# Optimization experiments

Measured on AMD Instinct MI355X. Metric: run time of the kernel, lower is better.

Reference implementation:

```python
import jax, jax.numpy as jnp
import numpy as np

B, N, D, H, C = 4, 1024, 768, 12, 3
Dh = D // H                      # 64
HID = int(D * 4.0 * (2.0 / 3.0)) # 2048 (SwiGLU hidden)
EPS = 1e-5


def layernorm(x, g, b):
    m = jnp.mean(x, axis=-1, keepdims=True)
    v = jnp.mean(jnp.square(x - m), axis=-1, keepdims=True)
    return (x - m) * jax.lax.rsqrt(v + EPS) * g + b


def setup_inputs() -> dict:
    key = jax.random.key(0)
    ks = jax.random.split(key, 8)
    x = jax.random.normal(ks[0], (B, N, D), jnp.float32)
    coords = jax.random.uniform(ks[1], (B, N, C), jnp.float32)
    qkv_w = jax.random.normal(ks[2], (3 * D, D), jnp.float32) * 0.02
    qkv_b = jnp.zeros((3 * D,), jnp.float32)
    rel_w = jax.random.normal(ks[3], (H, C), jnp.float32) * 0.1
    ln1_g = jnp.ones((D,), jnp.float32)
    ln1_b = jnp.zeros((D,), jnp.float32)
    ln2_g = jnp.ones((D,), jnp.float32)
    ln2_b = jnp.zeros((D,), jnp.float32)
    win_w = jax.random.normal(ks[4], (2 * HID, D), jnp.float32) * 0.02
    win_b = jnp.zeros((2 * HID,), jnp.float32)
    wout_w = jax.random.normal(ks[5], (D, HID), jnp.float32) * 0.02
    wout_b = jnp.zeros((D,), jnp.float32)
    return dict(x=x, coords=coords, ln1_g=ln1_g, ln1_b=ln1_b, qkv_w=qkv_w,
                qkv_b=qkv_b, rel_w=rel_w, ln2_g=ln2_g, ln2_b=ln2_b,
                win_w=win_w, win_b=win_b, wout_w=wout_w, wout_b=wout_b)


def reference(x, coords, ln1_g, ln1_b, qkv_w, qkv_b, rel_w, ln2_g, ln2_b,
              win_w, win_b, wout_w, wout_b):
    # --- PatchAttention on norm1(x) ---
    h = layernorm(x, ln1_g, ln1_b)
    qkv = h @ qkv_w.T + qkv_b                    # (B,N,3D)
    q, k, v = jnp.split(qkv, 3, axis=-1)

    def heads(t):  # (B,N,D) -> (B,H,N,Dh)
        return t.reshape(B, N, H, Dh).transpose(0, 2, 1, 3)

    qh, kh, vh = heads(q), heads(k), heads(v)
    scale = 1.0 / np.sqrt(Dh).astype(np.float32)
    scores = jnp.einsum('bhid,bhjd->bhij', qh, kh) * scale
    # coord bias: (coords_i - coords_j) . W_h  ==  p[b,h,i] - p[b,h,j]
    p = jnp.einsum('bnc,hc->bhn', coords, rel_w)  # (B,H,N)
    scores = scores + p[:, :, :, None] - p[:, :, None, :]
    attn = jax.nn.softmax(scores, axis=-1)
    o = jnp.einsum('bhij,bhjd->bhid', attn, vh)   # (B,H,N,Dh)
    o = o.transpose(0, 2, 1, 3).reshape(B, N, D)
    x = x + o

    # --- SwiGLU FFN on norm2(x) ---
    h2 = layernorm(x, ln2_g, ln2_b)
    uv = h2 @ win_w.T + win_b                     # (B,N,2*HID)
    u, g = jnp.split(uv, 2, axis=-1)
    act = jax.nn.silu(u) * g
    return x + act @ wout_w.T + wout_b
```

## Files before the change

kernel.cpp:

```cpp
#include <hip/hip_runtime.h>
#include <math.h>

typedef unsigned short u16;
typedef __bf16 bf16x8 __attribute__((ext_vector_type(8)));
typedef __bf16 bf16x4 __attribute__((ext_vector_type(4)));
typedef u16 u16x4 __attribute__((ext_vector_type(4)));
typedef float f32x4 __attribute__((ext_vector_type(4)));

#define NTOK 1024
#define DMODEL 768
#define NHEAD 12
#define LD3 2304
#define HIDDIM 2048

__device__ __forceinline__ float b2f(u16 u) {
  unsigned int t = ((unsigned int)u) << 16;
  float f;
  __builtin_memcpy(&f, &t, 4);
  return f;
}
__device__ __forceinline__ u16 f2b(float f) {
  unsigned int t;
  __builtin_memcpy(&t, &f, 4);
  t += 0x7fffu + ((t >> 16) & 1u);
  return (u16)(t >> 16);
}

__device__ __forceinline__ void gl_lds16(const u16* g, u16* l) {
  __builtin_amdgcn_global_load_lds(
      (__attribute__((address_space(1))) const unsigned int*)g,
      (__attribute__((address_space(3))) unsigned int*)l, 16, 0, 0);
}

__global__ __launch_bounds__(256) void signal_kernel(float* __restrict__ out,
                                                     int n, float c) {
  int i = blockIdx.x * 256 + threadIdx.x;
  if (i < n) out[i] = c;
}

__global__ __launch_bounds__(256) void detect_kernel(const u16* __restrict__ x,
                                                     int* __restrict__ flag) {
  __shared__ int cnt;
  if (threadIdx.x == 0) cnt = 0;
  __syncthreads();
  int bad = 0;
  for (int i = threadIdx.x; i < 4096; i += 256) {
    u16 v = x[2 * i];
    int e = (v >> 7) & 0xFF;
    if (e >= 0xC0) bad++;
  }
  atomicAdd(&cnt, bad);
  __syncthreads();
  if (threadIdx.x == 0) *flag = (cnt >= 64) ? 1 : 0;
}

struct CanonJobs {
  const void* s[13];
  u16* d[13];
  int n[13];
};

__global__ __launch_bounds__(256) void canon_kernel(CanonJobs jobs,
                                                    const int* __restrict__ flag) {
  int j = blockIdx.y;
  int n4 = jobs.n[j] >> 2;
  const void* s = jobs.s[j];
  u16* d = jobs.d[j];
  bool isf32 = (*flag != 0);
  for (int i = blockIdx.x * 256 + threadIdx.x; i < n4; i += gridDim.x * 256) {
    if (isf32) {
      f32x4 v = *((const f32x4*)s + i);
      u16x4 o = {f2b(v[0]), f2b(v[1]), f2b(v[2]), f2b(v[3])};
      *((u16x4*)d + i) = o;
    } else {
      *((u16x4*)d + i) = *((const u16x4*)s + i);
    }
  }
}

__global__ __launch_bounds__(256) void ln_bf16_kernel(
    const u16* __restrict__ x, const u16* __restrict__ g,
    const u16* __restrict__ b, u16* __restrict__ out) {
  int row = blockIdx.x;
  int tid = threadIdx.x;
  const u16* xr = x + (size_t)row * DMODEL;
  float v0 = b2f(xr[tid]), v1 = b2f(xr[tid + 256]), v2 = b2f(xr[tid + 512]);
  float s = v0 + v1 + v2;
  float q = v0 * v0 + v1 * v1 + v2 * v2;
#pragma unroll
  for (int off = 32; off; off >>= 1) {
    s += __shfl_xor(s, off, 64);
    q += __shfl_xor(q, off, 64);
  }
  __shared__ float rs[4], rq[4];
  int wv = tid >> 6;
  if ((tid & 63) == 0) { rs[wv] = s; rq[wv] = q; }
  __syncthreads();
  s = rs[0] + rs[1] + rs[2] + rs[3];
  q = rq[0] + rq[1] + rq[2] + rq[3];
  float mean = s * (1.0f / 768.0f);
  float var = q * (1.0f / 768.0f) - mean * mean;
  float inv = rsqrtf(var + 1e-5f);
  u16* outr = out + (size_t)row * DMODEL;
  outr[tid]       = f2b((v0 - mean) * inv * b2f(g[tid])       + b2f(b[tid]));
  outr[tid + 256] = f2b((v1 - mean) * inv * b2f(g[tid + 256]) + b2f(b[tid + 256]));
  outr[tid + 512] = f2b((v2 - mean) * inv * b2f(g[tid + 512]) + b2f(b[tid + 512]));
}

__global__ __launch_bounds__(256) void ln_f32_kernel(
    const float* __restrict__ x, const u16* __restrict__ g,
    const u16* __restrict__ b, u16* __restrict__ out) {
  int row = blockIdx.x;
  int tid = threadIdx.x;
  const float* xr = x + (size_t)row * DMODEL;
  float v0 = xr[tid], v1 = xr[tid + 256], v2 = xr[tid + 512];
  float s = v0 + v1 + v2;
  float q = v0 * v0 + v1 * v1 + v2 * v2;
#pragma unroll
  for (int off = 32; off; off >>= 1) {
    s += __shfl_xor(s, off, 64);
    q += __shfl_xor(q, off, 64);
  }
  __shared__ float rs[4], rq[4];
  int wv = tid >> 6;
  if ((tid & 63) == 0) { rs[wv] = s; rq[wv] = q; }
  __syncthreads();
  s = rs[0] + rs[1] + rs[2] + rs[3];
  q = rq[0] + rq[1] + rq[2] + rq[3];
  float mean = s * (1.0f / 768.0f);
  float var = q * (1.0f / 768.0f) - mean * mean;
  float inv = rsqrtf(var + 1e-5f);
  u16* outr = out + (size_t)row * DMODEL;
  outr[tid]       = f2b((v0 - mean) * inv * b2f(g[tid])       + b2f(b[tid]));
  outr[tid + 256] = f2b((v1 - mean) * inv * b2f(g[tid + 256]) + b2f(b[tid + 256]));
  outr[tid + 512] = f2b((v2 - mean) * inv * b2f(g[tid + 512]) + b2f(b[tid + 512]));
}

__global__ __launch_bounds__(256) void gemm_bt(
    const u16* __restrict__ Ap, const u16* __restrict__ Wp,
    const u16* __restrict__ bias, u16* __restrict__ Cp, int Nn, int K) {
  __shared__ __align__(16) u16 Al[3 * 128 * 32], Bl[3 * 64 * 32];
  int lane = threadIdx.x & 63;
  int wv = threadIdx.x >> 6;
  int q16 = lane & 15, quad = lane >> 4;
  int mB0 = blockIdx.y * 128;
  int nB0 = blockIdx.x * 64;
  int mW = (wv >> 1) * 64, nW = (wv & 1) * 32;
  int srow = lane >> 2;
  int scol = ((lane & 3) ^ ((lane >> 3) & 3)) * 8;
  int sx8 = (quad ^ ((q16 >> 1) & 3)) * 8;
  int r0 = wv * 32 + srow, r1 = r0 + 16;
  int rb = wv * 16 + srow;
  const u16* Ag0 = Ap + (size_t)(mB0 + r0) * K + scol;
  const u16* Ag1 = Ap + (size_t)(mB0 + r1) * K + scol;
  const u16* Wg  = Wp + (size_t)(nB0 + rb) * K + scol;
  int ch0 = wv * 1024, ch1 = ch0 + 512, chb = wv * 512;
  int nsteps = K >> 5;
  f32x4 acc[4][2] = {};
#pragma unroll
  for (int tt = 0; tt < 2; ++tt) {
    int k0 = tt * 32;
    gl_lds16(Ag0 + k0, Al + tt * 4096 + ch0);
    gl_lds16(Ag1 + k0, Al + tt * 4096 + ch1);
    gl_lds16(Wg + k0, Bl + tt * 2048 + chb);
  }
  int n3 = nsteps / 3;
  for (int kb = 0; kb < n3; ++kb) {
#pragma unroll
    for (int c = 0; c < 3; ++c) {
      int t = kb * 3 + c;
      if (t < nsteps - 1) asm volatile("s_waitcnt vmcnt(3)" ::: "memory");
      else                asm volatile("s_waitcnt vmcnt(0)" ::: "memory");
      __builtin_amdgcn_sched_barrier(0);
      __builtin_amdgcn_s_barrier();
      __builtin_amdgcn_sched_barrier(0);
      if (t < nsteps - 2) {
        int k0 = (t + 2) * 32;
        int bs = (c + 2) % 3;
        gl_lds16(Ag0 + k0, Al + bs * 4096 + ch0);
        gl_lds16(Ag1 + k0, Al + bs * 4096 + ch1);
        gl_lds16(Wg + k0, Bl + bs * 2048 + chb);
      }
      const __bf16* Ab = (const __bf16*)(Al + c * 4096);
      const __bf16* Bb = (const __bf16*)(Bl + c * 2048);
      bf16x8 af[4], bfr[2];
#pragma unroll
      for (int si = 0; si < 4; ++si)
        af[si] = *(const bf16x8*)(Ab + (mW + si * 16 + q16) * 32 + sx8);
#pragma unroll
      for (int sj = 0; sj < 2; ++sj)
        bfr[sj] = *(const bf16x8*)(Bb + (nW + sj * 16 + q16) * 32 + sx8);
#pragma unroll
      for (int si = 0; si < 4; ++si)
#pragma unroll
        for (int sj = 0; sj < 2; ++sj)
          acc[si][sj] = __builtin_amdgcn_mfma_f32_16x16x32_bf16(af[si], bfr[sj], acc[si][sj], 0, 0, 0);
    }
  }
#pragma unroll
  for (int si = 0; si < 4; ++si)
#pragma unroll
    for (int sj = 0; sj < 2; ++sj) {
      int col = nB0 + nW + sj * 16 + q16;
      float bcol = b2f(bias[col]);
#pragma unroll
      for (int r = 0; r < 4; ++r) {
        int rowi = mB0 + mW + si * 16 + quad * 4 + r;
        Cp[(size_t)rowi * Nn + col] = f2b(acc[si][sj][r] + bcol);
      }
    }
}

__global__ __launch_bounds__(256) void gemm_out_split(
    const u16* __restrict__ Ap, const u16* __restrict__ Wp,
    const u16* __restrict__ bias, const float* __restrict__ res,
    float* __restrict__ part, float* __restrict__ out) {
  __shared__ __align__(16) u16 Al[4 * 128 * 32], Bl[4 * 64 * 32];
  int lane = threadIdx.x & 63;
  int wv = threadIdx.x >> 6;
  int q16 = lane & 15, quad = lane >> 4;
  int mB0 = blockIdx.y * 128;
  int nB0 = blockIdx.x * 64;
  int kz = blockIdx.z;
  int kbase = kz * 1024;
  int mW = (wv >> 1) * 64, nW = (wv & 1) * 32;
  int srow = lane >> 2;
  int scol = ((lane & 3) ^ ((lane >> 3) & 3)) * 8;
  int sx8 = (quad ^ ((q16 >> 1) & 3)) * 8;
  int r0 = wv * 32 + srow, r1 = r0 + 16;
  int rb = wv * 16 + srow;
  const u16* Ag0 = Ap + (size_t)(mB0 + r0) * 2048 + kbase + scol;
  const u16* Ag1 = Ap + (size_t)(mB0 + r1) * 2048 + kbase + scol;
  const u16* Wg  = Wp + (size_t)(nB0 + rb) * 2048 + kbase + scol;
  int ch0 = wv * 1024, ch1 = ch0 + 512, chb = wv * 512;
  f32x4 acc[4][2] = {};
#pragma unroll
  for (int tt = 0; tt < 2; ++tt) {
    int k0 = tt * 32;
    gl_lds16(Ag0 + k0, Al + tt * 4096 + ch0);
    gl_lds16(Ag1 + k0, Al + tt * 4096 + ch1);
    gl_lds16(Wg + k0, Bl + tt * 2048 + chb);
  }
  for (int kb = 0; kb < 8; ++kb) {
#pragma unroll
    for (int c = 0; c < 4; ++c) {
      int t = kb * 4 + c;
      if (t < 31) asm volatile("s_waitcnt vmcnt(3)" ::: "memory");
      else        asm volatile("s_waitcnt vmcnt(0)" ::: "memory");
      __builtin_amdgcn_sched_barrier(0);
      __builtin_amdgcn_s_barrier();
      __builtin_amdgcn_sched_barrier(0);
      if (t < 30) {
        int k0 = (t + 2) * 32;
        int bs = (c + 2) & 3;
        gl_lds16(Ag0 + k0, Al + bs * 4096 + ch0);
        gl_lds16(Ag1 + k0, Al + bs * 4096 + ch1);
        gl_lds16(Wg + k0, Bl + bs * 2048 + chb);
      }
      const __bf16* Ab = (const __bf16*)(Al + c * 4096);
      const __bf16* Bb = (const __bf16*)(Bl + c * 2048);
      bf16x8 af[4], bfr[2];
#pragma unroll
      for (int si = 0; si < 4; ++si)
        af[si] = *(const bf16x8*)(Ab + (mW + si * 16 + q16) * 32 + sx8);
#pragma unroll
      for (int sj = 0; sj < 2; ++sj)
        bfr[sj] = *(const bf16x8*)(Bb + (nW + sj * 16 + q16) * 32 + sx8);
#pragma unroll
      for (int si = 0; si < 4; ++si)
#pragma unroll
        for (int sj = 0; sj < 2; ++sj)
          acc[si][sj] = __builtin_amdgcn_mfma_f32_16x16x32_bf16(af[si], bfr[sj], acc[si][sj], 0, 0, 0);
    }
  }
#pragma unroll
  for (int si = 0; si < 4; ++si)
#pragma unroll
    for (int sj = 0; sj < 2; ++sj) {
      int col = nB0 + nW + sj * 16 + q16;
#pragma unroll
      for (int r = 0; r < 4; ++r) {
        int rowi = mB0 + mW + si * 16 + quad * 4 + r;
        size_t idx = (size_t)rowi * 768 + col;
        if (kz == 0) {
          part[idx] = acc[si][sj][r];
        } else {
          out[idx] = acc[si][sj][r] + b2f(bias[col]) + res[idx];
        }
      }
    }
}

__global__ __launch_bounds__(256) void add_kernel(float* __restrict__ out,
                                                  const float* __restrict__ part) {
  int i = blockIdx.x * 256 + threadIdx.x;
  f32x4 o = ((f32x4*)out)[i];
  f32x4 p = ((const f32x4*)part)[i];
#pragma unroll
  for (int r = 0; r < 4; ++r) o[r] += p[r];
  ((f32x4*)out)[i] = o;
}

__global__ __launch_bounds__(256) void ffn_in_kernel(
    const u16* __restrict__ hp, const u16* __restrict__ Wp,
    const u16* __restrict__ bias, u16* __restrict__ actp) {
  __shared__ __align__(16) u16 Al[3 * 128 * 32], Bl[3 * 64 * 32];
  int lane = threadIdx.x & 63;
  int wv = threadIdx.x >> 6;
  int q16 = lane & 15, quad = lane >> 4;
  int mB0 = blockIdx.y * 128;
  int cB0 = blockIdx.x * 32;
  int mW = (wv >> 1) * 64;
  int cW = (wv & 1) * 16;
  int srow = lane >> 2;
  int scol = ((lane & 3) ^ ((lane >> 3) & 3)) * 8;
  int sx8 = (quad ^ ((q16 >> 1) & 3)) * 8;
  int r0 = wv * 32 + srow, r1 = r0 + 16;
  int rb = wv * 16 + srow;
  int gb = (rb < 32) ? (cB0 + rb) : (HIDDIM + cB0 + rb - 32);
  const u16* Ag0 = hp + (size_t)(mB0 + r0) * DMODEL + scol;
  const u16* Ag1 = hp + (size_t)(mB0 + r1) * DMODEL + scol;
  const u16* Wg  = Wp + (size_t)gb * DMODEL + scol;
  int ch0 = wv * 1024, ch1 = ch0 + 512, chb = wv * 512;
  f32x4 au[4] = {}, ag[4] = {};
#pragma unroll
  for (int tt = 0; tt < 2; ++tt) {
    int k0 = tt * 32;
    gl_lds16(Ag0 + k0, Al + tt * 4096 + ch0);
    gl_lds16(Ag1 + k0, Al + tt * 4096 + ch1);
    gl_lds16(Wg + k0, Bl + tt * 2048 + chb);
  }
  for (int kb = 0; kb < 8; ++kb) {
#pragma unroll
    for (int c = 0; c < 3; ++c) {
      int t = kb * 3 + c;
      if (t < 23) asm volatile("s_waitcnt vmcnt(3)" ::: "memory");
      else        asm volatile("s_waitcnt vmcnt(0)" ::: "memory");
      __builtin_amdgcn_sched_barrier(0);
      __builtin_amdgcn_s_barrier();
      __builtin_amdgcn_sched_barrier(0);
      if (t < 22) {
        int k0 = (t + 2) * 32;
        int bs = (c + 2) % 3;
        gl_lds16(Ag0 + k0, Al + bs * 4096 + ch0);
        gl_lds16(Ag1 + k0, Al + bs * 4096 + ch1);
        gl_lds16(Wg + k0, Bl + bs * 2048 + chb);
      }
      const __bf16* Ab = (const __bf16*)(Al + c * 4096);
      const __bf16* Bb = (const __bf16*)(Bl + c * 2048);
      bf16x8 af[4], wu, wg;
#pragma unroll
      for (int si = 0; si < 4; ++si)
        af[si] = *(const bf16x8*)(Ab + (mW + si * 16 + q16) * 32 + sx8);
      wu = *(const bf16x8*)(Bb + (cW + q16) * 32 + sx8);
      wg = *(const bf16x8*)(Bb + (32 + cW + q16) * 32 + sx8);
#pragma unroll
      for (int si = 0; si < 4; ++si) {
        au[si] = __builtin_amdgcn_mfma_f32_16x16x32_bf16(af[si], wu, au[si], 0, 0, 0);
        ag[si] = __builtin_amdgcn_mfma_f32_16x16x32_bf16(af[si], wg, ag[si], 0, 0, 0);
      }
    }
  }
  int col = cB0 + cW + q16;
  float bu = b2f(bias[col]);
  float bg = b2f(bias[HIDDIM + col]);
#pragma unroll
  for (int si = 0; si < 4; ++si) {
#pragma unroll
    for (int r = 0; r < 4; ++r) {
      int rowi = mB0 + mW + si * 16 + quad * 4 + r;
      float u = au[si][r] + bu;
      float g = ag[si][r] + bg;
      float s = u / (1.0f + __expf(-u));
      actp[(size_t)rowi * HIDDIM + col] = f2b(s * g);
    }
  }
}

__global__ __launch_bounds__(256) void p_kernel(
    const u16* __restrict__ coords, const u16* __restrict__ relw,
    float* __restrict__ p) {
  const float LOG2E = 1.4426950408889634f;
  int idx = blockIdx.x * 256 + threadIdx.x;
  float c0 = b2f(coords[idx * 3 + 0]);
  float c1 = b2f(coords[idx * 3 + 1]);
  float c2 = b2f(coords[idx * 3 + 2]);
  int b = idx >> 10, n = idx & 1023;
#pragma unroll
  for (int h = 0; h < NHEAD; ++h) {
    float w0 = b2f(relw[h * 3 + 0]), w1 = b2f(relw[h * 3 + 1]), w2 = b2f(relw[h * 3 + 2]);
    p[(size_t)(b * NHEAD + h) * NTOK + n] = (c0 * w0 + c1 * w1 + c2 * w2) * LOG2E;
  }
}

__global__ __launch_bounds__(256) void vt_kernel(const u16* __restrict__ qkvp,
                                                 u16* __restrict__ vtp) {
  int blk = blockIdx.x;
  int b = blk / 192;
  int rem = blk % 192;
  int h = rem >> 4;
  int nt = rem & 15;
  int wv = threadIdx.x >> 6;
  int d = threadIdx.x & 63;
  int n0 = nt * 64 + wv * 16;
  const u16* src = qkvp + ((size_t)(b * NTOK) + n0) * LD3 + 2 * DMODEL + h * 64 + d;
  u16* dst = vtp + ((size_t)((b * NHEAD + h) * 64 + d)) * NTOK + n0;
#pragma unroll
  for (int c = 0; c < 2; ++c) {
    u16 buf[8] __attribute__((aligned(16)));
#pragma unroll
    for (int i = 0; i < 8; ++i) buf[i] = src[(size_t)(c * 8 + i) * LD3];
    *(uint4*)(dst + c * 8) = *(const uint4*)buf;
  }
}

__global__ __launch_bounds__(256) void attn_kernel(
    const u16* __restrict__ qkvp, const u16* __restrict__ vtp,
    const float* __restrict__ p2, const u16* __restrict__ xp,
    float* __restrict__ x1) {
  const __bf16* qb = (const __bf16*)qkvp;
  __shared__ __align__(16) u16 Kl[4][32 * 64];
  __shared__ __align__(16) u16 Vl[4][64 * 32];
  __shared__ __align__(16) u16 Pl[4][16][40];
  __shared__ __align__(16) float Pb[1024];
  int lane = threadIdx.x & 63;
  int wv = threadIdx.x >> 6;
  int hw = blockIdx.x;
  int g = hw % 48;
  int nt = hw / 48;
  int b = g / 12, h = g % 12;
  int i0 = (nt * 4 + wv) * 16;
  int q16 = lane & 15, quad = lane >> 4;

  const float scl2 = 0.125f * 1.4426950408889634f;

  const __bf16* qrow = qb + ((size_t)(b * NTOK) + i0 + q16) * LD3 + h * 64;
  bf16x8 bq0 = *(const bf16x8*)(qrow + quad * 8);
  bf16x8 bq1 = *(const bf16x8*)(qrow + 32 + quad * 8);

  const float* prow = p2 + (size_t)(b * NHEAD + h) * NTOK;

  int krw = wv * 8 + (lane >> 3);
  int ks  = (lane & 7) ^ (krw & 7);
  const u16* kg0 = qkvp + (size_t)(b * NTOK) * LD3 + DMODEL + h * 64 + ks * 8;
  int vrw = wv * 16 + (lane >> 2);
  int vs  = (lane & 3) ^ ((vrw >> 1) & 3);
  const u16* vg0 = vtp + ((size_t)((b * NHEAD + h) * 64 + vrw)) * NTOK + vs * 8;

  int kx0 = (quad ^ (q16 & 7)) << 3;
  int kx1 = ((4 | quad) ^ (q16 & 7)) << 3;
  int vx  = (quad ^ ((q16 >> 1) & 3)) << 3;

  float mrun = -1e30f, lsum = 0.f;
  f32x4 accO[4] = {};

  gl_lds16((const u16*)(prow + wv * 256 + lane * 4), (u16*)&Pb[wv * 256]);
#pragma unroll
  for (int tt = 0; tt < 3; ++tt) {
    gl_lds16(kg0 + (size_t)(tt * 32 + krw) * LD3, &Kl[tt][wv * 512]);
    gl_lds16(vg0 + tt * 32, &Vl[tt][wv * 512]);
  }

  for (int kb = 0; kb < 8; ++kb) {
#pragma unroll
    for (int c = 0; c < 4; ++c) {
      int t = kb * 4 + c;
      if (t < 30)       asm volatile("s_waitcnt vmcnt(4)" ::: "memory");
      else if (t == 30) asm volatile("s_waitcnt vmcnt(2)" ::: "memory");
      else              asm volatile("s_waitcnt vmcnt(0)" ::: "memory");
      __builtin_amdgcn_sched_barrier(0);
      __builtin_amdgcn_s_barrier();
      __builtin_amdgcn_sched_barrier(0);
      if (t < 29) {
        int j = (t + 3) * 32;
        gl_lds16(kg0 + (size_t)(j + krw) * LD3, &Kl[(c + 3) & 3][wv * 512]);
        gl_lds16(vg0 + j, &Vl[(c + 3) & 3][wv * 512]);
      }

      int j0 = t * 32;
      const __bf16* Kb = (const __bf16*)Kl[c];
      bf16x8 ka00 = *(const bf16x8*)(Kb + q16 * 64 + kx0);
      bf16x8 ka01 = *(const bf16x8*)(Kb + q16 * 64 + kx1);
      bf16x8 ka10 = *(const bf16x8*)(Kb + (16 + q16) * 64 + kx0);
      bf16x8 ka11 = *(const bf16x8*)(Kb + (16 + q16) * 64 + kx1);
      f32x4 st0 = {}, st1 = {};
      st0 = __builtin_amdgcn_mfma_f32_16x16x32_bf16(ka00, bq0, st0, 0, 0, 0);
      st0 = __builtin_amdgcn_mfma_f32_16x16x32_bf16(ka01, bq1, st0, 0, 0, 0);
      st1 = __builtin_amdgcn_mfma_f32_16x16x32_bf16(ka10, bq0, st1, 0, 0, 0);
      st1 = __builtin_amdgcn_mfma_f32_16x16x32_bf16(ka11, bq1, st1, 0, 0, 0);

      f32x4 pjl = *(const f32x4*)(&Pb[j0 + 4 * quad]);
      f32x4 pjh = *(const f32x4*)(&Pb[j0 + 16 + 4 * quad]);
      float sl[4], sh[4];
#pragma unroll
      for (int r = 0; r < 4; ++r) {
        sl[r] = st0[r] * scl2 - pjl[r];
        sh[r] = st1[r] * scl2 - pjh[r];
      }
      float lm = fmaxf(fmaxf(fmaxf(sl[0], sl[1]), fmaxf(sl[2], sl[3])),
                       fmaxf(fmaxf(sh[0], sh[1]), fmaxf(sh[2], sh[3])));
      lm = fmaxf(lm, __shfl_xor(lm, 16, 64));
      lm = fmaxf(lm, __shfl_xor(lm, 32, 64));
      float mn = fmaxf(mrun, lm);
      float alpha = exp2f(mrun - mn);
      mrun = mn;
      float pl[4], ph[4];
#pragma unroll
      for (int r = 0; r < 4; ++r) {
        pl[r] = exp2f(sl[r] - mn);
        ph[r] = exp2f(sh[r] - mn);
      }
      float ts = (pl[0] + pl[1]) + (pl[2] + pl[3]) +
                 (ph[0] + ph[1]) + (ph[2] + ph[3]);
      ts += __shfl_xor(ts, 16, 64);
      ts += __shfl_xor(ts, 32, 64);
      lsum = lsum * alpha + ts;

      bf16x4 w0 = {(__bf16)pl[0], (__bf16)pl[1], (__bf16)pl[2], (__bf16)pl[3]};
      bf16x4 w1 = {(__bf16)ph[0], (__bf16)ph[1], (__bf16)ph[2], (__bf16)ph[3]};
      *(bf16x4*)(&Pl[wv][q16][4 * quad]) = w0;
      *(bf16x4*)(&Pl[wv][q16][16 + 4 * quad]) = w1;
      bf16x8 ap = *(const bf16x8*)(&Pl[wv][q16][quad * 8]);

      const __bf16* Vb = (const __bf16*)Vl[c];
#pragma unroll
      for (int ds = 0; ds < 4; ++ds) {
        bf16x8 av = *(const bf16x8*)(Vb + (ds * 16 + q16) * 32 + vx);
        f32x4 cc = accO[ds];
#pragma unroll
        for (int r = 0; r < 4; ++r) cc[r] *= alpha;
        accO[ds] = __builtin_amdgcn_mfma_f32_16x16x32_bf16(av, ap, cc, 0, 0, 0);
      }
    }
  }

  float rl = 1.0f / lsum;
  size_t rowbase = ((size_t)(b * NTOK) + i0 + q16) * DMODEL + h * 64;
#pragma unroll
  for (int ds = 0; ds < 4; ++ds) {
    int d0 = ds * 16 + quad * 4;
    u16x4 xv = *(const u16x4*)(xp + rowbase + d0);
    f32x4 ov;
#pragma unroll
    for (int r = 0; r < 4; ++r) ov[r] = b2f(xv[r]) + accO[ds][r] * rl;
    *(f32x4*)(x1 + rowbase + d0) = ov;
  }
}

extern "C" void kernel_launch(void* const* d_in, const int* in_sizes, int n_in,
                              void* d_out, int out_size, void* d_ws, size_t ws_size,
                              hipStream_t stream) {
  static const int esz[13] = {3145728, 12288, 768, 768, 1769472, 2304, 36,
                              768, 768, 3145728, 4096, 1572864, 768};
  float sig = -1.f;
  if (n_in != 13) {
    sig = 6000.f + 100.f * (float)n_in;
  } else {
    for (int i = 0; i < 13; ++i)
      if (in_sizes[i] != esz[i]) { sig = 1000.f + 100.f * (float)i; break; }
  }
  if (sig < 0.f && ws_size < 57258496ULL) sig = 3000.f;
  if (sig < 0.f && out_size != 3145728) sig = 3100.f;
  if (sig >= 0.f) {
    signal_kernel<<<(out_size + 255) / 256, 256, 0, stream>>>((float*)d_out, out_size, sig);
    return;
  }

  char* ws = (char*)d_ws;
  int*  flag    = (int*)ws;
  u16*  cx      = (u16*)(ws + 256);
  u16*  cqkvw   = (u16*)(ws + 6291712);
  u16*  cwinw   = (u16*)(ws + 9830656);
  u16*  cwoutw  = (u16*)(ws + 16122112);
  u16*  ccoords = (u16*)(ws + 19267840);
  u16*  cln1g   = (u16*)(ws + 19292416);
  u16*  cln1b   = (u16*)(ws + 19293952);
  u16*  cqkvb   = (u16*)(ws + 19295488);
  u16*  crelw   = (u16*)(ws + 19300096);
  u16*  cln2g   = (u16*)(ws + 19300352);
  u16*  cln2b   = (u16*)(ws + 19301888);
  u16*  cwinb   = (u16*)(ws + 19303424);
  u16*  cwoutb  = (u16*)(ws + 19311616);
  u16*  h       = (u16*)(ws + 19313152);
  u16*  qkv     = (u16*)(ws + 25604608);
  float* pbuf   = (float*)(ws + 44478976);
  float* x1     = (float*)(ws + 44675584);
  u16*  act     = qkv;
  u16*  vt      = h;
  float* part   = (float*)(ws + 256);

  detect_kernel<<<1, 256, 0, stream>>>((const u16*)d_in[0], flag);

  CanonJobs jobs;
  u16* dsts[13] = {cx, ccoords, cln1g, cln1b, cqkvw, cqkvb, crelw,
                   cln2g, cln2b, cwinw, cwinb, cwoutw, cwoutb};
  for (int i = 0; i < 13; ++i) {
    jobs.s[i] = d_in[i];
    jobs.d[i] = dsts[i];
    jobs.n[i] = in_sizes[i];
  }
  canon_kernel<<<dim3(768, 13), 256, 0, stream>>>(jobs, flag);

  ln_bf16_kernel<<<4096, 256, 0, stream>>>(cx, cln1g, cln1b, h);
  gemm_bt<<<dim3(36, 32), 256, 0, stream>>>(h, cqkvw, cqkvb, qkv, 2304, 768);
  p_kernel<<<16, 256, 0, stream>>>(ccoords, crelw, pbuf);
  vt_kernel<<<768, 256, 0, stream>>>(qkv, vt);
  attn_kernel<<<768, 256, 0, stream>>>(qkv, vt, pbuf, cx, x1);
  ln_f32_kernel<<<4096, 256, 0, stream>>>(x1, cln2g, cln2b, h);
  ffn_in_kernel<<<dim3(64, 32), 256, 0, stream>>>(h, cwinw, cwinb, act);
  gemm_out_split<<<dim3(12, 32, 2), 256, 0, stream>>>(act, cwoutw, cwoutb, x1,
                                                      part, (float*)d_out);
  add_kernel<<<3072, 256, 0, stream>>>((float*)d_out, part);
}
```

Before: 292.0 us.

## Cut kernel launches: fold detection, p-bias, split-K; deepen FFN pipeline

Removes the separate detect kernel by having each canon block sample the input and ballot-count the exponent bits itself. The coordinate-bias kernel is merged into the V-transpose kernel. The split-K output GEMM plus its add kernel become one 64x64-tile GEMM with a 3-stage prefetch. The FFN-in GEMM's LDS ring goes from 3 to 6 stages with a prefetch distance of 5. Together these cut launch count and partial-sum traffic, at the cost of more LDS per block, lower occupancy, and a smaller detection sample.

```diff
diff --git a/kernel.cpp b/kernel.cpp
--- a/kernel.cpp
+++ b/kernel.cpp
@@ -38,39 +38,31 @@
   if (i < n) out[i] = c;
 }
 
-__global__ __launch_bounds__(256) void detect_kernel(const u16* __restrict__ x,
-                                                     int* __restrict__ flag) {
-  __shared__ int cnt;
-  if (threadIdx.x == 0) cnt = 0;
-  __syncthreads();
-  int bad = 0;
-  for (int i = threadIdx.x; i < 4096; i += 256) {
-    u16 v = x[2 * i];
-    int e = (v >> 7) & 0xFF;
-    if (e >= 0xC0) bad++;
-  }
-  atomicAdd(&cnt, bad);
-  __syncthreads();
-  if (threadIdx.x == 0) *flag = (cnt >= 64) ? 1 : 0;
-}
-
 struct CanonJobs {
   const void* s[13];
   u16* d[13];
   int n[13];
 };
 
-__global__ __launch_bounds__(256) void canon_kernel(CanonJobs jobs,
-                                                    const int* __restrict__ flag) {
+__global__ __launch_bounds__(256) void canon_kernel(CanonJobs jobs) {
+  __shared__ int csh;
+  u16 v = ((const u16*)jobs.s[0])[2 * threadIdx.x];
+  int e = (v >> 7) & 0xFF;
+  unsigned long long m = __ballot(e >= 0xC0);
+  if (threadIdx.x == 0) csh = 0;
+  __syncthreads();
+  if ((threadIdx.x & 63) == 0) atomicAdd(&csh, __popcll(m));
+  __syncthreads();
+  bool isf32 = csh >= 8;
+
   int j = blockIdx.y;
   int n4 = jobs.n[j] >> 2;
   const void* s = jobs.s[j];
   u16* d = jobs.d[j];
-  bool isf32 = (*flag != 0);
   for (int i = blockIdx.x * 256 + threadIdx.x; i < n4; i += gridDim.x * 256) {
     if (isf32) {
-      f32x4 v = *((const f32x4*)s + i);
-      u16x4 o = {f2b(v[0]), f2b(v[1]), f2b(v[2]), f2b(v[3])};
+      f32x4 vv = *((const f32x4*)s + i);
+      u16x4 o = {f2b(vv[0]), f2b(vv[1]), f2b(vv[2]), f2b(vv[3])};
       *((u16x4*)d + i) = o;
     } else {
       *((u16x4*)d + i) = *((const u16x4*)s + i);
@@ -211,100 +203,81 @@
     }
 }
 
-__global__ __launch_bounds__(256) void gemm_out_split(
+__global__ __launch_bounds__(256) void gemm_out_f32(
     const u16* __restrict__ Ap, const u16* __restrict__ Wp,
     const u16* __restrict__ bias, const float* __restrict__ res,
-    float* __restrict__ part, float* __restrict__ out) {
-  __shared__ __align__(16) u16 Al[4 * 128 * 32], Bl[4 * 64 * 32];
+    float* __restrict__ out) {
+  __shared__ __align__(16) u16 Al[4 * 64 * 32], Bl[4 * 64 * 32];
   int lane = threadIdx.x & 63;
   int wv = threadIdx.x >> 6;
   int q16 = lane & 15, quad = lane >> 4;
-  int mB0 = blockIdx.y * 128;
+  int mB0 = blockIdx.y * 64;
   int nB0 = blockIdx.x * 64;
-  int kz = blockIdx.z;
-  int kbase = kz * 1024;
-  int mW = (wv >> 1) * 64, nW = (wv & 1) * 32;
+  int mW = (wv >> 1) * 32, nW = (wv & 1) * 32;
   int srow = lane >> 2;
   int scol = ((lane & 3) ^ ((lane >> 3) & 3)) * 8;
   int sx8 = (quad ^ ((q16 >> 1) & 3)) * 8;
-  int r0 = wv * 32 + srow, r1 = r0 + 16;
-  int rb = wv * 16 + srow;
-  const u16* Ag0 = Ap + (size_t)(mB0 + r0) * 2048 + kbase + scol;
-  const u16* Ag1 = Ap + (size_t)(mB0 + r1) * 2048 + kbase + scol;
-  const u16* Wg  = Wp + (size_t)(nB0 + rb) * 2048 + kbase + scol;
-  int ch0 = wv * 1024, ch1 = ch0 + 512, chb = wv * 512;
-  f32x4 acc[4][2] = {};
-#pragma unroll
-  for (int tt = 0; tt < 2; ++tt) {
-    int k0 = tt * 32;
-    gl_lds16(Ag0 + k0, Al + tt * 4096 + ch0);
-    gl_lds16(Ag1 + k0, Al + tt * 4096 + ch1);
-    gl_lds16(Wg + k0, Bl + tt * 2048 + chb);
-  }
-  for (int kb = 0; kb < 8; ++kb) {
+  int ra = wv * 16 + srow;
+  const u16* Ag = Ap + (size_t)(mB0 + ra) * 2048 + scol;
+  const u16* Wg = Wp + (size_t)(nB0 + ra) * 2048 + scol;
+  int ch = wv * 512;
+  f32x4 acc[2][2] = {};
+#pragma unroll
+  for (int tt = 0; tt < 3; ++tt) {
+    gl_lds16(Ag + tt * 32, Al + tt * 2048 + ch);
+    gl_lds16(Wg + tt * 32, Bl + tt * 2048 + ch);
+  }
+  for (int kb = 0; kb < 16; ++kb) {
 #pragma unroll
     for (int c = 0; c < 4; ++c) {
       int t = kb * 4 + c;
-      if (t < 31) asm volatile("s_waitcnt vmcnt(3)" ::: "memory");
-      else        asm volatile("s_waitcnt vmcnt(0)" ::: "memory");
+      if (t < 62)       asm volatile("s_waitcnt vmcnt(4)" ::: "memory");
+      else if (t == 62) asm volatile("s_waitcnt vmcnt(2)" ::: "memory");
+      else              asm volatile("s_waitcnt vmcnt(0)" ::: "memory");
       __builtin_amdgcn_sched_barrier(0);
       __builtin_amdgcn_s_barrier();
       __builtin_amdgcn_sched_barrier(0);
-      if (t < 30) {
-        int k0 = (t + 2) * 32;
-        int bs = (c + 2) & 3;
-        gl_lds16(Ag0 + k0, Al + bs * 4096 + ch0);
-        gl_lds16(Ag1 + k0, Al + bs * 4096 + ch1);
-        gl_lds16(Wg + k0, Bl + bs * 2048 + chb);
-      }
-      const __bf16* Ab = (const __bf16*)(Al + c * 4096);
+      if (t < 61) {
+        int k0 = (t + 3) * 32;
+        int bs = (c + 3) & 3;
+        gl_lds16(Ag + k0, Al + bs * 2048 + ch);
+        gl_lds16(Wg + k0, Bl + bs * 2048 + ch);
+      }
+      const __bf16* Ab = (const __bf16*)(Al + c * 2048);
       const __bf16* Bb = (const __bf16*)(Bl + c * 2048);
-      bf16x8 af[4], bfr[2];
-#pragma unroll
-      for (int si = 0; si < 4; ++si)
+      bf16x8 af[2], bfr[2];
+#pragma unroll
+      for (int si = 0; si < 2; ++si)
         af[si] = *(const bf16x8*)(Ab + (mW + si * 16 + q16) * 32 + sx8);
 #pragma unroll
       for (int sj = 0; sj < 2; ++sj)
         bfr[sj] = *(const bf16x8*)(Bb + (nW + sj * 16 + q16) * 32 + sx8);
 #pragma unroll
-      for (int si = 0; si < 4; ++si)
+      for (int si = 0; si < 2; ++si)
 #pragma unroll
         for (int sj = 0; sj < 2; ++sj)
           acc[si][sj] = __builtin_amdgcn_mfma_f32_16x16x32_bf16(af[si], bfr[sj], acc[si][sj], 0, 0, 0);
     }
   }
 #pragma unroll
-  for (int si = 0; si < 4; ++si)
+  for (int si = 0; si < 2; ++si)
 #pragma unroll
     for (int sj = 0; sj < 2; ++sj) {
       int col = nB0 + nW + sj * 16 + q16;
+      float bcol = b2f(bias[col]);
 #pragma unroll
       for (int r = 0; r < 4; ++r) {
         int rowi = mB0 + mW + si * 16 + quad * 4 + r;
         size_t idx = (size_t)rowi * 768 + col;
-        if (kz == 0) {
-          part[idx] = acc[si][sj][r];
-        } else {
-          out[idx] = acc[si][sj][r] + b2f(bias[col]) + res[idx];
-        }
-      }
-    }
-}
-
-__global__ __launch_bounds__(256) void add_kernel(float* __restrict__ out,
-                                                  const float* __restrict__ part) {
-  int i = blockIdx.x * 256 + threadIdx.x;
-  f32x4 o = ((f32x4*)out)[i];
-  f32x4 p = ((const f32x4*)part)[i];
-#pragma unroll
-  for (int r = 0; r < 4; ++r) o[r] += p[r];
-  ((f32x4*)out)[i] = o;
+        out[idx] = acc[si][sj][r] + bcol + res[idx];
+      }
+    }
 }
 
 __global__ __launch_bounds__(256) void ffn_in_kernel(
     const u16* __restrict__ hp, const u16* __restrict__ Wp,
     const u16* __restrict__ bias, u16* __restrict__ actp) {
-  __shared__ __align__(16) u16 Al[3 * 128 * 32], Bl[3 * 64 * 32];
+  __shared__ __align__(16) u16 Al[6 * 128 * 32], Bl[6 * 64 * 32];
   int lane = threadIdx.x & 63;
   int wv = threadIdx.x >> 6;
   int q16 = lane & 15, quad = lane >> 4;
@@ -324,24 +297,27 @@
   int ch0 = wv * 1024, ch1 = ch0 + 512, chb = wv * 512;
   f32x4 au[4] = {}, ag[4] = {};
 #pragma unroll
-  for (int tt = 0; tt < 2; ++tt) {
+  for (int tt = 0; tt < 5; ++tt) {
     int k0 = tt * 32;
     gl_lds16(Ag0 + k0, Al + tt * 4096 + ch0);
     gl_lds16(Ag1 + k0, Al + tt * 4096 + ch1);
     gl_lds16(Wg + k0, Bl + tt * 2048 + chb);
   }
-  for (int kb = 0; kb < 8; ++kb) {
-#pragma unroll
-    for (int c = 0; c < 3; ++c) {
-      int t = kb * 3 + c;
-      if (t < 23) asm volatile("s_waitcnt vmcnt(3)" ::: "memory");
-      else        asm volatile("s_waitcnt vmcnt(0)" ::: "memory");
+  for (int kb = 0; kb < 4; ++kb) {
+#pragma unroll
+    for (int c = 0; c < 6; ++c) {
+      int t = kb * 6 + c;
+      if (t < 20)       asm volatile("s_waitcnt vmcnt(12)" ::: "memory");
+      else if (t == 20) asm volatile("s_waitcnt vmcnt(9)" ::: "memory");
+      else if (t == 21) asm volatile("s_waitcnt vmcnt(6)" ::: "memory");
+      else if (t == 22) asm volatile("s_waitcnt vmcnt(3)" ::: "memory");
+      else              asm volatile("s_waitcnt vmcnt(0)" ::: "memory");
       __builtin_amdgcn_sched_barrier(0);
       __builtin_amdgcn_s_barrier();
       __builtin_amdgcn_sched_barrier(0);
-      if (t < 22) {
-        int k0 = (t + 2) * 32;
-        int bs = (c + 2) % 3;
+      if (t < 19) {
+        int k0 = (t + 5) * 32;
+        int bs = (c + 5) % 6;
         gl_lds16(Ag0 + k0, Al + bs * 4096 + ch0);
         gl_lds16(Ag1 + k0, Al + bs * 4096 + ch1);
         gl_lds16(Wg + k0, Bl + bs * 2048 + chb);
@@ -377,24 +353,11 @@
   }
 }
 
-__global__ __launch_bounds__(256) void p_kernel(
-    const u16* __restrict__ coords, const u16* __restrict__ relw,
-    float* __restrict__ p) {
-  const float LOG2E = 1.4426950408889634f;
-  int idx = blockIdx.x * 256 + threadIdx.x;
-  float c0 = b2f(coords[idx * 3 + 0]);
-  float c1 = b2f(coords[idx * 3 + 1]);
-  float c2 = b2f(coords[idx * 3 + 2]);
-  int b = idx >> 10, n = idx & 1023;
-#pragma unroll
-  for (int h = 0; h < NHEAD; ++h) {
-    float w0 = b2f(relw[h * 3 + 0]), w1 = b2f(relw[h * 3 + 1]), w2 = b2f(relw[h * 3 + 2]);
-    p[(size_t)(b * NHEAD + h) * NTOK + n] = (c0 * w0 + c1 * w1 + c2 * w2) * LOG2E;
-  }
-}
-
 __global__ __launch_bounds__(256) void vt_kernel(const u16* __restrict__ qkvp,
-                                                 u16* __restrict__ vtp) {
+                                                 u16* __restrict__ vtp,
+                                                 const u16* __restrict__ coords,
+                                                 const u16* __restrict__ relw,
+                                                 float* __restrict__ p) {
   int blk = blockIdx.x;
   int b = blk / 192;
   int rem = blk % 192;
@@ -411,6 +374,18 @@
 #pragma unroll
     for (int i = 0; i < 8; ++i) buf[i] = src[(size_t)(c * 8 + i) * LD3];
     *(uint4*)(dst + c * 8) = *(const uint4*)buf;
+  }
+  if (nt == 0) {
+    const float LOG2E = 1.4426950408889634f;
+    float w0 = b2f(relw[h * 3 + 0]), w1 = b2f(relw[h * 3 + 1]), w2 = b2f(relw[h * 3 + 2]);
+    float* prow = p + (size_t)(b * NHEAD + h) * NTOK;
+    for (int n = threadIdx.x; n < NTOK; n += 256) {
+      int idx = b * NTOK + n;
+      float c0 = b2f(coords[idx * 3 + 0]);
+      float c1 = b2f(coords[idx * 3 + 1]);
+      float c2 = b2f(coords[idx * 3 + 2]);
+      prow[n] = (c0 * w0 + c1 * w1 + c2 * w2) * LOG2E;
+    }
   }
 }
 
@@ -567,7 +542,6 @@
   }
 
   char* ws = (char*)d_ws;
-  int*  flag    = (int*)ws;
   u16*  cx      = (u16*)(ws + 256);
   u16*  cqkvw   = (u16*)(ws + 6291712);
   u16*  cwinw   = (u16*)(ws + 9830656);
@@ -587,9 +561,6 @@
   float* x1     = (float*)(ws + 44675584);
   u16*  act     = qkv;
   u16*  vt      = h;
-  float* part   = (float*)(ws + 256);
-
-  detect_kernel<<<1, 256, 0, stream>>>((const u16*)d_in[0], flag);
 
   CanonJobs jobs;
   u16* dsts[13] = {cx, ccoords, cln1g, cln1b, cqkvw, cqkvb, crelw,
@@ -599,16 +570,14 @@
     jobs.d[i] = dsts[i];
     jobs.n[i] = in_sizes[i];
   }
-  canon_kernel<<<dim3(768, 13), 256, 0, stream>>>(jobs, flag);
+  canon_kernel<<<dim3(768, 13), 256, 0, stream>>>(jobs);
 
   ln_bf16_kernel<<<4096, 256, 0, stream>>>(cx, cln1g, cln1b, h);
   gemm_bt<<<dim3(36, 32), 256, 0, stream>>>(h, cqkvw, cqkvb, qkv, 2304, 768);
-  p_kernel<<<16, 256, 0, stream>>>(ccoords, crelw, pbuf);
-  vt_kernel<<<768, 256, 0, stream>>>(qkv, vt);
+  vt_kernel<<<768, 256, 0, stream>>>(qkv, vt, ccoords, crelw, pbuf);
   attn_kernel<<<768, 256, 0, stream>>>(qkv, vt, pbuf, cx, x1);
   ln_f32_kernel<<<4096, 256, 0, stream>>>(x1, cln2g, cln2b, h);
   ffn_in_kernel<<<dim3(64, 32), 256, 0, stream>>>(h, cwinw, cwinb, act);
-  gemm_out_split<<<dim3(12, 32, 2), 256, 0, stream>>>(act, cwoutw, cwoutb, x1,
-                                                      part, (float*)d_out);
-  add_kernel<<<3072, 256, 0, stream>>>((float*)d_out, part);
-}
+  gemm_out_f32<<<dim3(12, 64), 256, 0, stream>>>(act, cwoutw, cwoutb, x1,
+                                                 (float*)d_out);
+}
```

Result: no change. 287.2 us (-1.7%).
